# Kernel optimization log

Hardware: AMD Instinct MI355X
Metric: run time of the kernel (lower is better)

Reference implementation:

```python
import jax, jax.numpy as jnp
import numpy as np

B, T, D, U = 32, 2048, 1024, 1024

def setup_inputs() -> dict:
    key = jax.random.key(0)
    ks = jax.random.split(key, 6)
    scale = 1.0 / np.sqrt(D)
    return {
        "features": jax.random.normal(ks[0], (B, T, D), dtype=jnp.float32),
        "hidden": jax.random.normal(ks[1], (B, D), dtype=jnp.float32),
        "W1": jax.random.normal(ks[2], (D, U), dtype=jnp.float32) * scale,
        "b1": jnp.zeros((U,), dtype=jnp.float32),
        "W2": jax.random.normal(ks[3], (D, U), dtype=jnp.float32) * scale,
        "b2": jnp.zeros((U,), dtype=jnp.float32),
        "V": jax.random.normal(ks[4], (U, 1), dtype=jnp.float32) * (1.0 / np.sqrt(U)),
        "bV": jnp.zeros((1,), dtype=jnp.float32),
    }

def reference(features, hidden, W1, b1, W2, b2, V, bV):
    # features: [B,T,D], hidden: [B,D]
    proj_f = jnp.einsum('btd,du->btu', features, W1) + b1          # [B,T,U]
    proj_h = (hidden @ W2 + b2)[:, None, :]                        # [B,1,U]
    score = jnp.tanh(proj_f + proj_h)                              # [B,T,U]
    logits = jnp.einsum('btu,uo->bto', score, V) + bV              # [B,T,1]
    attention_weights = jax.nn.softmax(logits, axis=1)             # [B,T,1]
    context_vector = jnp.sum(attention_weights * features, axis=1) # [B,D]
    return context_vector, attention_weights
```

## Files before the change

### kernel.cpp

```cpp
#include <hip/hip_runtime.h>
#include <hip/hip_bf16.h>
#include <hip/hip_fp16.h>

#define B_ 32
#define T_ 2048
#define D_ 1024
#define U_ 1024
#define M_ (B_ * T_)
#define NT_ 4

typedef _Float16 f16x8 __attribute__((ext_vector_type(8)));
typedef _Float16 f16x4 __attribute__((ext_vector_type(4)));
typedef float f32x4 __attribute__((ext_vector_type(4)));

__device__ __forceinline__ float fast_tanh(float x) {
    float xc = fminf(fmaxf(x, -10.f), 10.f);
    float e = __expf(2.f * xc);
    return 1.f - 2.f / (e + 1.f);
}

__device__ __forceinline__ void load_lds16(const void* g, void* l) {
    __builtin_amdgcn_global_load_lds(
        (const __attribute__((address_space(1))) void*)g,
        (__attribute__((address_space(3))) void*)l, 16, 0, 0);
}

__global__ void precast_kernel(const float* __restrict__ in,
                               _Float16* __restrict__ out) {
    size_t i = (size_t)blockIdx.x * 256 + threadIdx.x;
    const size_t stride = (size_t)2048 * 256;
    const size_t n8 = (size_t)M_ * D_ / 8;
    for (size_t j = i; j < n8; j += stride) {
        f32x4 a = *(const f32x4*)(in + j * 8);
        f32x4 b = *(const f32x4*)(in + j * 8 + 4);
        f16x8 h;
        h[0] = (_Float16)a[0]; h[1] = (_Float16)a[1];
        h[2] = (_Float16)a[2]; h[3] = (_Float16)a[3];
        h[4] = (_Float16)b[0]; h[5] = (_Float16)b[1];
        h[6] = (_Float16)b[2]; h[7] = (_Float16)b[3];
        *(f16x8*)(out + j * 8) = h;
    }
}

__global__ void transpose_cast_kernel(const float* __restrict__ W1,
                                      _Float16* __restrict__ W1t) {
    int u = blockIdx.x * 256 + threadIdx.x;
    int d0 = blockIdx.y * 64;
    for (int j8 = 0; j8 < 8; ++j8) {
        f16x8 h;
        #pragma unroll
        for (int j = 0; j < 8; ++j)
            h[j] = (_Float16)W1[(size_t)(d0 + j8 * 8 + j) * U_ + u];
        *(f16x8*)&W1t[(size_t)u * D_ + d0 + j8 * 8] = h;
    }
}

__global__ void proj_h_partial_kernel(const float* __restrict__ hidden,
                                      const float* __restrict__ W2,
                                      float* __restrict__ pph) {
    int u = blockIdx.x * 256 + threadIdx.x;
    int c = blockIdx.y;
    __shared__ float hb[32][128];
    for (int i = threadIdx.x; i < 32 * 128; i += 256)
        hb[i >> 7][i & 127] = hidden[(i >> 7) * D_ + c * 128 + (i & 127)];
    __syncthreads();
    float acc[32] = {};
    for (int d = 0; d < 128; ++d) {
        float w = W2[(size_t)(c * 128 + d) * U_ + u];
        #pragma unroll
        for (int b = 0; b < 32; ++b) acc[b] = fmaf(hb[b][d], w, acc[b]);
    }
    #pragma unroll
    for (int b = 0; b < 32; ++b)
        pph[((size_t)c * 32 + b) * U_ + u] = acc[b];
}

__global__ void proj_h_combine_kernel(const float* __restrict__ pph,
                                      const float* __restrict__ b1,
                                      const float* __restrict__ b2,
                                      float* __restrict__ ph) {
    int u = blockIdx.x * 256 + threadIdx.x;
    float bias = b1[u] + b2[u];
    for (int b = 0; b < 32; ++b) {
        float s = bias;
        #pragma unroll
        for (int c = 0; c < 8; ++c) s += pph[((size_t)c * 32 + b) * U_ + u];
        ph[b * U_ + u] = s;
    }
}


#define VM4 asm volatile("s_waitcnt vmcnt(4)" ::: "memory");
#define VM0 asm volatile("s_waitcnt vmcnt(0)" ::: "memory");

#define STAGE_A(bb, kh, kof) \
    load_lds16(pA + (kof) + (kh) * 64, sb + (bb) * 65536 + (kh) * 16384 + tid * 16); \
    load_lds16(pA + (size_t)128 * D_ * 2 + (kof) + (kh) * 64, \
               sb + (bb) * 65536 + (kh) * 16384 + 8192 + tid * 16);
#define STAGE_B(bb, kh, kof) \
    load_lds16(pB + (kof) + (kh) * 64, sb + (bb) * 65536 + 32768 + (kh) * 16384 + tid * 16); \
    load_lds16(pB + (size_t)128 * D_ * 2 + (kof) + (kh) * 64, \
               sb + (bb) * 65536 + 32768 + (kh) * 16384 + 8192 + tid * 16);

#define PH(curv, kh, mh, STG, WAITV) do { \
    const char* base_ = sb + (curv) * 65536 + (kh) * 16384; \
    if ((mh) == 0) { \
        _Pragma("unroll") \
        for (int n_ = 0; n_ < 4; ++n_) \
            bf[n_] = *(const f16x8*)(base_ + 32768 + wc * 4096 + n_ * 1024 + laneOff); \
    } \
    _Pragma("unroll") \
    for (int m_ = 0; m_ < 4; ++m_) \
        af[m_] = *(const f16x8*)(base_ + wr * 8192 + (mh) * 4096 + m_ * 1024 + laneOff); \
    STG \
    __builtin_amdgcn_sched_barrier(0); \
    WAITV \
    __builtin_amdgcn_sched_barrier(0); \
    __builtin_amdgcn_s_barrier(); \
    asm volatile("s_waitcnt lgkmcnt(0)" ::: "memory"); \
    __builtin_amdgcn_sched_barrier(0); \
    __builtin_amdgcn_s_setprio(1); \
    _Pragma("unroll") \
    for (int m_ = 0; m_ < 4; ++m_) { \
        _Pragma("unroll") \
        for (int n_ = 0; n_ < 4; ++n_) \
            acc[(mh) * 4 + m_][n_] = __builtin_amdgcn_mfma_f32_16x16x32_f16( \
                af[m_], bf[n_], acc[(mh) * 4 + m_][n_], 0, 0, 0); \
    } \
    __builtin_amdgcn_s_setprio(0); \
    __builtin_amdgcn_sched_barrier(0); \
    __builtin_amdgcn_s_barrier(); \
    __builtin_amdgcn_sched_barrier(0); \
} while (0)

__global__ __launch_bounds__(512, 2)
void gemm_logits_8ph_kernel(const _Float16* __restrict__ A,
                            const _Float16* __restrict__ Bt,
                            const float* __restrict__ ph,
                            const float* __restrict__ V,
                            float* __restrict__ part)
{
    __shared__ __align__(16) char smem_raw[131072];
    char* sb = smem_raw;

    int bid = blockIdx.x;
    int xcd = bid & 7, local = bid >> 3;
    int mt = xcd * 32 + (local >> 2);
    int nt = local & 3;

    int tid = threadIdx.x;
    int l = tid & 63, wid = tid >> 6;
    int wr = wid >> 2, wc = wid & 3;
    int lrow = l & 15;

    const _Float16* Ag = A + (size_t)mt * 256 * D_;
    const _Float16* Bg = Bt + (size_t)nt * 256 * D_;

    int srow = tid >> 2;
    int chunk = (tid & 3) ^ ((srow >> 1) & 3);
    size_t rb = (size_t)srow * (D_ * 2) + (size_t)chunk * 16;
    const char* pA = (const char*)Ag + rb;
    const char* pB = (const char*)Bg + rb;

    int laneOff = lrow * 64 + (((l >> 4) ^ ((lrow >> 1) & 3)) << 4);

    f32x4 acc[8][4] = {};
    f16x8 af[4], bf[4];

    STAGE_A(0, 0, 0)
    STAGE_B(0, 0, 0)
    STAGE_A(0, 1, 0)
    STAGE_B(0, 1, 0)
    VM4
    __builtin_amdgcn_s_barrier();
    __builtin_amdgcn_sched_barrier(0);

    #pragma unroll 1
    for (int t = 0; t < 15; ++t) {
        int cur = t & 1, nxt = cur ^ 1;
        int kof = (t + 1) * 128;
        PH(cur, 0, 0, STAGE_A(nxt, 0, kof), );
        PH(cur, 0, 1, STAGE_B(nxt, 0, kof), VM4);
        PH(cur, 1, 0, STAGE_A(nxt, 1, kof), );
        PH(cur, 1, 1, STAGE_B(nxt, 1, kof), VM4);
    }
    PH(1, 0, 0, , );
    PH(1, 0, 1, , VM0);
    PH(1, 1, 0, , );
    PH(1, 1, 1, , );

    int bidx = mt >> 3;
    const float* phb = ph + bidx * U_;
    float Vv[4], phv[4];
    #pragma unroll
    for (int n = 0; n < 4; ++n) {
        int u = nt * 256 + wc * 64 + n * 16 + lrow;
        Vv[n] = V[u];
        phv[n] = phb[u];
    }
    float* lbuf = (float*)smem_raw;
    #pragma unroll
    for (int mh = 0; mh < 2; ++mh) {
        #pragma unroll
        for (int m = 0; m < 4; ++m) {
            #pragma unroll
            for (int r = 0; r < 4; ++r) {
                float p = 0.f;
                #pragma unroll
                for (int n = 0; n < 4; ++n) {
                    float s = fast_tanh(acc[mh * 4 + m][n][r] + phv[n]);
                    p = fmaf(s, Vv[n], p);
                }
                #pragma unroll
                for (int off = 1; off < 16; off <<= 1)
                    p += __shfl_xor(p, off, 64);
                if (lrow == 0) {
                    int row = wr * 128 + mh * 64 + m * 16 + ((l >> 4) << 2) + r;
                    lbuf[wc * 256 + row] = p;
                }
            }
        }
    }
    __syncthreads();
    if (tid < 256) {
        float v = lbuf[tid] + lbuf[256 + tid] + lbuf[512 + tid] + lbuf[768 + tid];
        part[(size_t)nt * M_ + mt * 256 + tid] = v;
    }
}

__global__ void softmax_kernel(const float* __restrict__ part,
                               float* __restrict__ wout) {
    int b = blockIdx.x;
    int tid = threadIdx.x;
    __shared__ float red[8];
    float lg[8];
    #pragma unroll
    for (int j = 0; j < 8; ++j) {
        int t = tid + j * 256;
        float s = 0.f;
        #pragma unroll
        for (int p = 0; p < NT_; ++p)
            s += part[(size_t)p * M_ + b * T_ + t];
        lg[j] = s;
    }
    float mx = lg[0];
    #pragma unroll
    for (int j = 1; j < 8; ++j) mx = fmaxf(mx, lg[j]);
    #pragma unroll
    for (int off = 1; off < 64; off <<= 1) mx = fmaxf(mx, __shfl_xor(mx, off, 64));
    int wv = tid >> 6;
    if ((tid & 63) == 0) red[wv] = mx;
    __syncthreads();
    mx = fmaxf(fmaxf(red[0], red[1]), fmaxf(red[2], red[3]));
    float e[8];
    float sum = 0.f;
    #pragma unroll
    for (int j = 0; j < 8; ++j) { e[j] = __expf(lg[j] - mx); sum += e[j]; }
    #pragma unroll
    for (int off = 1; off < 64; off <<= 1) sum += __shfl_xor(sum, off, 64);
    if ((tid & 63) == 0) red[4 + wv] = sum;
    __syncthreads();
    sum = red[4] + red[5] + red[6] + red[7];
    float inv = 1.f / sum;
    #pragma unroll
    for (int j = 0; j < 8; ++j)
        wout[b * T_ + tid + j * 256] = e[j] * inv;
}

#define TCH 128
__global__ void context_partial_f16_kernel(const _Float16* __restrict__ feats,
                                           const float* __restrict__ w,
                                           float* __restrict__ cpart) {
    int b = blockIdx.x, tc = blockIdx.y, tid = threadIdx.x;
    f32x4 acc = {0.f, 0.f, 0.f, 0.f};
    const _Float16* f = feats + ((size_t)b * T_ + tc * TCH) * D_ + tid * 4;
    const float* wp = w + b * T_ + tc * TCH;
    #pragma unroll 4
    for (int t = 0; t < TCH; ++t) {
        float wt = wp[t];
        f16x4 fv = *(const f16x4*)(f + (size_t)t * D_);
        acc[0] = fmaf(wt, (float)fv[0], acc[0]);
        acc[1] = fmaf(wt, (float)fv[1], acc[1]);
        acc[2] = fmaf(wt, (float)fv[2], acc[2]);
        acc[3] = fmaf(wt, (float)fv[3], acc[3]);
    }
    *(f32x4*)&cpart[((size_t)tc * B_ + b) * D_ + tid * 4] = acc;
}

__global__ void context_reduce_kernel(const float* __restrict__ cpart,
                                      float* __restrict__ out) {
    int i = blockIdx.x * 256 + threadIdx.x;
    float s = 0.f;
    #pragma unroll
    for (int tc = 0; tc < 16; ++tc)
        s += cpart[(size_t)tc * (B_ * D_) + i];
    out[i] = s;
}

extern "C" void kernel_launch(void* const* d_in, const int* in_sizes, int n_in,
                              void* d_out, int out_size, void* d_ws, size_t ws_size,
                              hipStream_t stream) {
    const float* features = (const float*)d_in[0];
    const float* hidden   = (const float*)d_in[1];
    const float* W1       = (const float*)d_in[2];
    const float* b1       = (const float*)d_in[3];
    const float* W2       = (const float*)d_in[4];
    const float* b2       = (const float*)d_in[5];
    const float* V        = (const float*)d_in[6];

    float* ctx_out = (float*)d_out;
    float* w_out   = ctx_out + B_ * D_;

    char* ws = (char*)d_ws;
    _Float16* W1t  = (_Float16*)ws;
    float* ph      = (float*)(ws + (size_t)(2 << 20));
    float* pph     = (float*)(ws + (size_t)(3 << 20));
    float* part    = (float*)(ws + (size_t)(4 << 20));
    float* cpart   = (float*)(ws + (size_t)(6 << 20));
    _Float16* featH = (_Float16*)(ws + (size_t)(8 << 20));

    transpose_cast_kernel<<<dim3(4, 16), 256, 0, stream>>>(W1, W1t);
    proj_h_partial_kernel<<<dim3(4, 8), 256, 0, stream>>>(hidden, W2, pph);
    proj_h_combine_kernel<<<4, 256, 0, stream>>>(pph, b1, b2, ph);
    precast_kernel<<<2048, 256, 0, stream>>>(features, featH);

    gemm_logits_8ph_kernel<<<(M_ / 256) * (U_ / 256), 512, 0, stream>>>(
        featH, W1t, ph, V, part);

    softmax_kernel<<<B_, 256, 0, stream>>>(part, w_out);
    context_partial_f16_kernel<<<dim3(B_, 16), 256, 0, stream>>>(featH, w_out, cpart);
    context_reduce_kernel<<<(B_ * D_) / 256, 256, 0, stream>>>(cpart, ctx_out);
}
```

Before: 318.4 us.

## Fuse fp32-to-fp16 feature cast into GEMM A-tile loading and drop precast

Removes the separate precast kernel that wrote an fp16 copy of the features. The GEMM now loads fp32 features into registers, converts them to fp16 and writes them into swizzled LDS, while W1t is still loaded asynchronously into LDS. The main loop is restructured into one double-buffered 64-wide K step per iteration with a single barrier. The context kernel now reads the fp32 features directly. This saves the precast's full read and write pass, but doubles the bytes read by the context kernel and adds register staging and conversion work inside the GEMM, which may weaken load/compute overlap.

```diff
diff --git a/kernel.cpp b/kernel.cpp
--- a/kernel.cpp
+++ b/kernel.cpp
@@ -10,7 +10,6 @@
 #define NT_ 4
 
 typedef _Float16 f16x8 __attribute__((ext_vector_type(8)));
-typedef _Float16 f16x4 __attribute__((ext_vector_type(4)));
 typedef float f32x4 __attribute__((ext_vector_type(4)));
 
 __device__ __forceinline__ float fast_tanh(float x) {
@@ -23,23 +22,6 @@
     __builtin_amdgcn_global_load_lds(
         (const __attribute__((address_space(1))) void*)g,
         (__attribute__((address_space(3))) void*)l, 16, 0, 0);
-}
-
-__global__ void precast_kernel(const float* __restrict__ in,
-                               _Float16* __restrict__ out) {
-    size_t i = (size_t)blockIdx.x * 256 + threadIdx.x;
-    const size_t stride = (size_t)2048 * 256;
-    const size_t n8 = (size_t)M_ * D_ / 8;
-    for (size_t j = i; j < n8; j += stride) {
-        f32x4 a = *(const f32x4*)(in + j * 8);
-        f32x4 b = *(const f32x4*)(in + j * 8 + 4);
-        f16x8 h;
-        h[0] = (_Float16)a[0]; h[1] = (_Float16)a[1];
-        h[2] = (_Float16)a[2]; h[3] = (_Float16)a[3];
-        h[4] = (_Float16)b[0]; h[5] = (_Float16)b[1];
-        h[6] = (_Float16)b[2]; h[7] = (_Float16)b[3];
-        *(f16x8*)(out + j * 8) = h;
-    }
 }
 
 __global__ void transpose_cast_kernel(const float* __restrict__ W1,
@@ -90,58 +72,46 @@
 }
 
 
-#define VM4 asm volatile("s_waitcnt vmcnt(4)" ::: "memory");
-#define VM0 asm volatile("s_waitcnt vmcnt(0)" ::: "memory");
-
-#define STAGE_A(bb, kh, kof) \
-    load_lds16(pA + (kof) + (kh) * 64, sb + (bb) * 65536 + (kh) * 16384 + tid * 16); \
-    load_lds16(pA + (size_t)128 * D_ * 2 + (kof) + (kh) * 64, \
-               sb + (bb) * 65536 + (kh) * 16384 + 8192 + tid * 16);
-#define STAGE_B(bb, kh, kof) \
-    load_lds16(pB + (kof) + (kh) * 64, sb + (bb) * 65536 + 32768 + (kh) * 16384 + tid * 16); \
-    load_lds16(pB + (size_t)128 * D_ * 2 + (kof) + (kh) * 64, \
-               sb + (bb) * 65536 + 32768 + (kh) * 16384 + 8192 + tid * 16);
-
-#define PH(curv, kh, mh, STG, WAITV) do { \
-    const char* base_ = sb + (curv) * 65536 + (kh) * 16384; \
-    if ((mh) == 0) { \
-        _Pragma("unroll") \
-        for (int n_ = 0; n_ < 4; ++n_) \
-            bf[n_] = *(const f16x8*)(base_ + 32768 + wc * 4096 + n_ * 1024 + laneOff); \
-    } \
-    _Pragma("unroll") \
-    for (int m_ = 0; m_ < 4; ++m_) \
-        af[m_] = *(const f16x8*)(base_ + wr * 8192 + (mh) * 4096 + m_ * 1024 + laneOff); \
-    STG \
-    __builtin_amdgcn_sched_barrier(0); \
-    WAITV \
-    __builtin_amdgcn_sched_barrier(0); \
-    __builtin_amdgcn_s_barrier(); \
-    asm volatile("s_waitcnt lgkmcnt(0)" ::: "memory"); \
-    __builtin_amdgcn_sched_barrier(0); \
-    __builtin_amdgcn_s_setprio(1); \
-    _Pragma("unroll") \
-    for (int m_ = 0; m_ < 4; ++m_) { \
-        _Pragma("unroll") \
-        for (int n_ = 0; n_ < 4; ++n_) \
-            acc[(mh) * 4 + m_][n_] = __builtin_amdgcn_mfma_f32_16x16x32_f16( \
-                af[m_], bf[n_], acc[(mh) * 4 + m_][n_], 0, 0, 0); \
-    } \
-    __builtin_amdgcn_s_setprio(0); \
-    __builtin_amdgcn_sched_barrier(0); \
-    __builtin_amdgcn_s_barrier(); \
-    __builtin_amdgcn_sched_barrier(0); \
+#define ISSUE_A(koff) do { \
+    const float* a0_ = pA0 + (koff); \
+    const float* a1_ = pA1 + (koff); \
+    araw0 = *(const f32x4*)(a0_);      araw1 = *(const f32x4*)(a0_ + 4); \
+    araw2 = *(const f32x4*)(a0_ + 8);  araw3 = *(const f32x4*)(a0_ + 12); \
+    araw4 = *(const f32x4*)(a1_);      araw5 = *(const f32x4*)(a1_ + 4); \
+    araw6 = *(const f32x4*)(a1_ + 8);  araw7 = *(const f32x4*)(a1_ + 12); \
 } while (0)
 
+#define ISSUE_B(koffb, bufoff) do { \
+    load_lds16(pB + 0 * 131072 + (koffb), smem + (bufoff) + 32768 + 0 * 8192 + tid * 16); \
+    load_lds16(pB + 1 * 131072 + (koffb), smem + (bufoff) + 32768 + 1 * 8192 + tid * 16); \
+    load_lds16(pB + 2 * 131072 + (koffb), smem + (bufoff) + 32768 + 2 * 8192 + tid * 16); \
+    load_lds16(pB + 3 * 131072 + (koffb), smem + (bufoff) + 32768 + 3 * 8192 + tid * 16); \
+} while (0)
+
+#define WRITE_A(nbptr) do { \
+    f16x8 h0_, h1_, h2_, h3_; \
+    h0_[0]=(_Float16)araw0[0]; h0_[1]=(_Float16)araw0[1]; h0_[2]=(_Float16)araw0[2]; h0_[3]=(_Float16)araw0[3]; \
+    h0_[4]=(_Float16)araw1[0]; h0_[5]=(_Float16)araw1[1]; h0_[6]=(_Float16)araw1[2]; h0_[7]=(_Float16)araw1[3]; \
+    h1_[0]=(_Float16)araw2[0]; h1_[1]=(_Float16)araw2[1]; h1_[2]=(_Float16)araw2[2]; h1_[3]=(_Float16)araw2[3]; \
+    h1_[4]=(_Float16)araw3[0]; h1_[5]=(_Float16)araw3[1]; h1_[6]=(_Float16)araw3[2]; h1_[7]=(_Float16)araw3[3]; \
+    h2_[0]=(_Float16)araw4[0]; h2_[1]=(_Float16)araw4[1]; h2_[2]=(_Float16)araw4[2]; h2_[3]=(_Float16)araw4[3]; \
+    h2_[4]=(_Float16)araw5[0]; h2_[5]=(_Float16)araw5[1]; h2_[6]=(_Float16)araw5[2]; h2_[7]=(_Float16)araw5[3]; \
+    h3_[0]=(_Float16)araw6[0]; h3_[1]=(_Float16)araw6[1]; h3_[2]=(_Float16)araw6[2]; h3_[3]=(_Float16)araw6[3]; \
+    h3_[4]=(_Float16)araw7[0]; h3_[5]=(_Float16)araw7[1]; h3_[6]=(_Float16)araw7[2]; h3_[7]=(_Float16)araw7[3]; \
+    *(f16x8*)((nbptr) + aw00) = h0_; \
+    *(f16x8*)((nbptr) + aw01) = h1_; \
+    *(f16x8*)((nbptr) + aw10) = h2_; \
+    *(f16x8*)((nbptr) + aw11) = h3_; \
+} while (0)
+
 __global__ __launch_bounds__(512, 2)
-void gemm_logits_8ph_kernel(const _Float16* __restrict__ A,
-                            const _Float16* __restrict__ Bt,
-                            const float* __restrict__ ph,
-                            const float* __restrict__ V,
-                            float* __restrict__ part)
+void gemm_logits_v4_kernel(const float* __restrict__ A,
+                           const _Float16* __restrict__ Bt,
+                           const float* __restrict__ ph,
+                           const float* __restrict__ V,
+                           float* __restrict__ part)
 {
-    __shared__ __align__(16) char smem_raw[131072];
-    char* sb = smem_raw;
+    __shared__ __align__(16) char smem[131072];
 
     int bid = blockIdx.x;
     int xcd = bid & 7, local = bid >> 3;
@@ -151,43 +121,78 @@
     int tid = threadIdx.x;
     int l = tid & 63, wid = tid >> 6;
     int wr = wid >> 2, wc = wid & 3;
-    int lrow = l & 15;
-
-    const _Float16* Ag = A + (size_t)mt * 256 * D_;
+    int lrow = l & 15, lksl = l >> 4;
+
+    const float* Ag = A + (size_t)mt * 256 * D_;
     const _Float16* Bg = Bt + (size_t)nt * 256 * D_;
 
-    int srow = tid >> 2;
-    int chunk = (tid & 3) ^ ((srow >> 1) & 3);
-    size_t rb = (size_t)srow * (D_ * 2) + (size_t)chunk * 16;
-    const char* pA = (const char*)Ag + rb;
-    const char* pB = (const char*)Bg + rb;
-
-    int laneOff = lrow * 64 + (((l >> 4) ^ ((lrow >> 1) & 3)) << 4);
+    const float* pA0 = Ag + (size_t)(tid >> 2) * D_ + (tid & 3) * 16;
+    const float* pA1 = pA0 + (size_t)128 * D_;
+    int c2 = (tid & 3) * 2;
+    int r0 = tid >> 2;
+    int sw = r0 & 7;
+    int aw00 = r0 * 128 + ((c2 ^ sw) << 4);
+    int aw01 = r0 * 128 + (((c2 | 1) ^ sw) << 4);
+    int aw10 = (r0 + 128) * 128 + ((c2 ^ sw) << 4);
+    int aw11 = (r0 + 128) * 128 + (((c2 | 1) ^ sw) << 4);
+
+    int bchunk = (tid & 7) ^ ((tid >> 3) & 7);
+    const char* pB = (const char*)Bg + (size_t)(tid >> 3) * 2048 + bchunk * 16;
+
+    int rowA = (wr * 128 + lrow) * 128;
+    int rowB = 32768 + (wc * 64 + lrow) * 128;
+    int sw7 = lrow & 7;
 
     f32x4 acc[8][4] = {};
-    f16x8 af[4], bf[4];
-
-    STAGE_A(0, 0, 0)
-    STAGE_B(0, 0, 0)
-    STAGE_A(0, 1, 0)
-    STAGE_B(0, 1, 0)
-    VM4
+    f32x4 araw0, araw1, araw2, araw3, araw4, araw5, araw6, araw7;
+
+    ISSUE_A(0);
+    ISSUE_B(0, 0);
+    WRITE_A(smem);
+    __builtin_amdgcn_sched_barrier(0);
+    asm volatile("s_waitcnt vmcnt(0)" ::: "memory");
+    asm volatile("s_waitcnt lgkmcnt(0)" ::: "memory");
+    __builtin_amdgcn_sched_barrier(0);
     __builtin_amdgcn_s_barrier();
     __builtin_amdgcn_sched_barrier(0);
 
     #pragma unroll 1
-    for (int t = 0; t < 15; ++t) {
-        int cur = t & 1, nxt = cur ^ 1;
-        int kof = (t + 1) * 128;
-        PH(cur, 0, 0, STAGE_A(nxt, 0, kof), );
-        PH(cur, 0, 1, STAGE_B(nxt, 0, kof), VM4);
-        PH(cur, 1, 0, STAGE_A(nxt, 1, kof), );
-        PH(cur, 1, 1, STAGE_B(nxt, 1, kof), VM4);
-    }
-    PH(1, 0, 0, , );
-    PH(1, 0, 1, , VM0);
-    PH(1, 1, 0, , );
-    PH(1, 1, 1, , );
+    for (int t = 0; t < 16; ++t) {
+        const char* bb = smem + (t & 1) * 65536;
+        char* nb = smem + ((t & 1) ^ 1) * 65536;
+        if (t < 15) {
+            ISSUE_A((t + 1) * 64);
+            ISSUE_B((t + 1) * 128, ((t & 1) ^ 1) * 65536);
+        }
+        __builtin_amdgcn_s_setprio(1);
+        #pragma unroll
+        for (int kh = 0; kh < 2; ++kh) {
+            int us = (((kh << 2) | lksl) ^ sw7) << 4;
+            f16x8 af[8], bf[4];
+            #pragma unroll
+            for (int n = 0; n < 4; ++n)
+                bf[n] = *(const f16x8*)(bb + rowB + n * 2048 + us);
+            #pragma unroll
+            for (int m = 0; m < 8; ++m)
+                af[m] = *(const f16x8*)(bb + rowA + m * 2048 + us);
+            #pragma unroll
+            for (int m = 0; m < 8; ++m)
+                #pragma unroll
+                for (int n = 0; n < 4; ++n)
+                    acc[m][n] = __builtin_amdgcn_mfma_f32_16x16x32_f16(
+                        af[m], bf[n], acc[m][n], 0, 0, 0);
+        }
+        __builtin_amdgcn_s_setprio(0);
+        if (t < 15) {
+            WRITE_A(nb);
+            __builtin_amdgcn_sched_barrier(0);
+            asm volatile("s_waitcnt vmcnt(0)" ::: "memory");
+            asm volatile("s_waitcnt lgkmcnt(0)" ::: "memory");
+            __builtin_amdgcn_sched_barrier(0);
+            __builtin_amdgcn_s_barrier();
+            __builtin_amdgcn_sched_barrier(0);
+        }
+    }
 
     int bidx = mt >> 3;
     const float* phb = ph + bidx * U_;
@@ -198,26 +203,23 @@
         Vv[n] = V[u];
         phv[n] = phb[u];
     }
-    float* lbuf = (float*)smem_raw;
-    #pragma unroll
-    for (int mh = 0; mh < 2; ++mh) {
-        #pragma unroll
-        for (int m = 0; m < 4; ++m) {
-            #pragma unroll
-            for (int r = 0; r < 4; ++r) {
-                float p = 0.f;
-                #pragma unroll
-                for (int n = 0; n < 4; ++n) {
-                    float s = fast_tanh(acc[mh * 4 + m][n][r] + phv[n]);
-                    p = fmaf(s, Vv[n], p);
-                }
-                #pragma unroll
-                for (int off = 1; off < 16; off <<= 1)
-                    p += __shfl_xor(p, off, 64);
-                if (lrow == 0) {
-                    int row = wr * 128 + mh * 64 + m * 16 + ((l >> 4) << 2) + r;
-                    lbuf[wc * 256 + row] = p;
-                }
+    float* lbuf = (float*)smem;
+    #pragma unroll
+    for (int m = 0; m < 8; ++m) {
+        #pragma unroll
+        for (int r = 0; r < 4; ++r) {
+            float p = 0.f;
+            #pragma unroll
+            for (int n = 0; n < 4; ++n) {
+                float s = fast_tanh(acc[m][n][r] + phv[n]);
+                p = fmaf(s, Vv[n], p);
+            }
+            #pragma unroll
+            for (int off = 1; off < 16; off <<= 1)
+                p += __shfl_xor(p, off, 64);
+            if (lrow == 0) {
+                int row = wr * 128 + m * 16 + ((l >> 4) << 2) + r;
+                lbuf[wc * 256 + row] = p;
             }
         }
     }
@@ -268,21 +270,20 @@
 }
 
 #define TCH 128
-__global__ void context_partial_f16_kernel(const _Float16* __restrict__ feats,
-                                           const float* __restrict__ w,
-                                           float* __restrict__ cpart) {
+__global__ void context_partial_kernel(const float* __restrict__ feats,
+                                       const float* __restrict__ w,
+                                       float* __restrict__ cpart) {
     int b = blockIdx.x, tc = blockIdx.y, tid = threadIdx.x;
     f32x4 acc = {0.f, 0.f, 0.f, 0.f};
-    const _Float16* f = feats + ((size_t)b * T_ + tc * TCH) * D_ + tid * 4;
+    const float* f = feats + ((size_t)b * T_ + tc * TCH) * D_ + tid * 4;
     const float* wp = w + b * T_ + tc * TCH;
-    #pragma unroll 4
     for (int t = 0; t < TCH; ++t) {
         float wt = wp[t];
-        f16x4 fv = *(const f16x4*)(f + (size_t)t * D_);
-        acc[0] = fmaf(wt, (float)fv[0], acc[0]);
-        acc[1] = fmaf(wt, (float)fv[1], acc[1]);
-        acc[2] = fmaf(wt, (float)fv[2], acc[2]);
-        acc[3] = fmaf(wt, (float)fv[3], acc[3]);
+        f32x4 fv = *(const f32x4*)(f + (size_t)t * D_);
+        acc[0] = fmaf(wt, fv[0], acc[0]);
+        acc[1] = fmaf(wt, fv[1], acc[1]);
+        acc[2] = fmaf(wt, fv[2], acc[2]);
+        acc[3] = fmaf(wt, fv[3], acc[3]);
     }
     *(f32x4*)&cpart[((size_t)tc * B_ + b) * D_ + tid * 4] = acc;
 }
@@ -312,22 +313,20 @@
     float* w_out   = ctx_out + B_ * D_;
 
     char* ws = (char*)d_ws;
-    _Float16* W1t  = (_Float16*)ws;
-    float* ph      = (float*)(ws + (size_t)(2 << 20));
-    float* pph     = (float*)(ws + (size_t)(3 << 20));
-    float* part    = (float*)(ws + (size_t)(4 << 20));
-    float* cpart   = (float*)(ws + (size_t)(6 << 20));
-    _Float16* featH = (_Float16*)(ws + (size_t)(8 << 20));
+    _Float16* W1t = (_Float16*)ws;
+    float* ph     = (float*)(ws + (size_t)(2 << 20));
+    float* pph    = (float*)(ws + (size_t)(3 << 20));
+    float* part   = (float*)(ws + (size_t)(4 << 20));
+    float* cpart  = (float*)(ws + (size_t)(6 << 20));
 
     transpose_cast_kernel<<<dim3(4, 16), 256, 0, stream>>>(W1, W1t);
     proj_h_partial_kernel<<<dim3(4, 8), 256, 0, stream>>>(hidden, W2, pph);
     proj_h_combine_kernel<<<4, 256, 0, stream>>>(pph, b1, b2, ph);
-    precast_kernel<<<2048, 256, 0, stream>>>(features, featH);
-
-    gemm_logits_8ph_kernel<<<(M_ / 256) * (U_ / 256), 512, 0, stream>>>(
-        featH, W1t, ph, V, part);
+
+    gemm_logits_v4_kernel<<<(M_ / 256) * (U_ / 256), 512, 0, stream>>>(
+        features, W1t, ph, V, part);
 
     softmax_kernel<<<B_, 256, 0, stream>>>(part, w_out);
-    context_partial_f16_kernel<<<dim3(B_, 16), 256, 0, stream>>>(featH, w_out, cpart);
+    context_partial_kernel<<<dim3(B_, 16), 256, 0, stream>>>(features, w_out, cpart);
     context_reduce_kernel<<<(B_ * D_) / 256, 256, 0, stream>>>(cpart, ctx_out);
 }
```

New measurement: 297.1 us. 1.07x faster.

## Pre-swizzle features and W1 into MFMA fragment layout, keep W1 slice resident in LDS

Applied to the files above, without the earlier changes.

Features and W1 are cast to fp16 and stored in a tiled layout that matches the MFMA 16x16x32 operand fragments. Each GEMM block now keeps a 64-column slice of W1 resident in LDS for the whole K range, while A fragments are loaded straight from global memory into registers with software double-buffering. Because block output tiles narrow from 256 to 64 columns, NT_ grows to 16 partial logit rows. The context kernel reads the same tiled layout and reduces with shuffles, which removes the separate context reduce kernel. This drops the per-K-step LDS staging and barriers for A, but each A tile is re-read from global memory by 16 column blocks, and occupancy is limited by the large LDS buffer.

```diff
diff --git a/kernel.cpp b/kernel.cpp
--- a/kernel.cpp
+++ b/kernel.cpp
@@ -7,10 +7,9 @@
 #define D_ 1024
 #define U_ 1024
 #define M_ (B_ * T_)
-#define NT_ 4
+#define NT_ 16
 
 typedef _Float16 f16x8 __attribute__((ext_vector_type(8)));
-typedef _Float16 f16x4 __attribute__((ext_vector_type(4)));
 typedef float f32x4 __attribute__((ext_vector_type(4)));
 
 __device__ __forceinline__ float fast_tanh(float x) {
@@ -25,33 +24,38 @@
         (__attribute__((address_space(3))) void*)l, 16, 0, 0);
 }
 
-__global__ void precast_kernel(const float* __restrict__ in,
-                               _Float16* __restrict__ out) {
-    size_t i = (size_t)blockIdx.x * 256 + threadIdx.x;
-    const size_t stride = (size_t)2048 * 256;
-    const size_t n8 = (size_t)M_ * D_ / 8;
-    for (size_t j = i; j < n8; j += stride) {
-        f32x4 a = *(const f32x4*)(in + j * 8);
-        f32x4 b = *(const f32x4*)(in + j * 8 + 4);
+__global__ void precastT_kernel(const float* __restrict__ in,
+                                _Float16* __restrict__ out) {
+    int mt = blockIdx.x;
+    int t = threadIdx.x;
+    int slot = t & 15, kb0 = t >> 4;
+    const float* src = in + ((size_t)mt * 16 + slot) * D_;
+    _Float16* dst = out + (size_t)mt * 16384 + slot * 8;
+    #pragma unroll
+    for (int i = 0; i < 8; ++i) {
+        int kb = kb0 + i * 16;
+        f32x4 a = *(const f32x4*)(src + kb * 8);
+        f32x4 b = *(const f32x4*)(src + kb * 8 + 4);
         f16x8 h;
         h[0] = (_Float16)a[0]; h[1] = (_Float16)a[1];
         h[2] = (_Float16)a[2]; h[3] = (_Float16)a[3];
         h[4] = (_Float16)b[0]; h[5] = (_Float16)b[1];
         h[6] = (_Float16)b[2]; h[7] = (_Float16)b[3];
-        *(f16x8*)(out + j * 8) = h;
-    }
-}
-
-__global__ void transpose_cast_kernel(const float* __restrict__ W1,
-                                      _Float16* __restrict__ W1t) {
+        *(f16x8*)(dst + kb * 128) = h;
+    }
+}
+
+__global__ void transpose_cast_W1T_kernel(const float* __restrict__ W1,
+                                          _Float16* __restrict__ W1T) {
     int u = blockIdx.x * 256 + threadIdx.x;
     int d0 = blockIdx.y * 64;
+    _Float16* dst = W1T + (size_t)(u >> 4) * 16384 + (u & 15) * 8;
     for (int j8 = 0; j8 < 8; ++j8) {
         f16x8 h;
         #pragma unroll
         for (int j = 0; j < 8; ++j)
             h[j] = (_Float16)W1[(size_t)(d0 + j8 * 8 + j) * U_ + u];
-        *(f16x8*)&W1t[(size_t)u * D_ + d0 + j8 * 8] = h;
+        *(f16x8*)(dst + (size_t)(d0 / 8 + j8) * 128) = h;
     }
 }
 
@@ -90,141 +94,111 @@
 }
 
 
-#define VM4 asm volatile("s_waitcnt vmcnt(4)" ::: "memory");
-#define VM0 asm volatile("s_waitcnt vmcnt(0)" ::: "memory");
-
-#define STAGE_A(bb, kh, kof) \
-    load_lds16(pA + (kof) + (kh) * 64, sb + (bb) * 65536 + (kh) * 16384 + tid * 16); \
-    load_lds16(pA + (size_t)128 * D_ * 2 + (kof) + (kh) * 64, \
-               sb + (bb) * 65536 + (kh) * 16384 + 8192 + tid * 16);
-#define STAGE_B(bb, kh, kof) \
-    load_lds16(pB + (kof) + (kh) * 64, sb + (bb) * 65536 + 32768 + (kh) * 16384 + tid * 16); \
-    load_lds16(pB + (size_t)128 * D_ * 2 + (kof) + (kh) * 64, \
-               sb + (bb) * 65536 + 32768 + (kh) * 16384 + 8192 + tid * 16);
-
-#define PH(curv, kh, mh, STG, WAITV) do { \
-    const char* base_ = sb + (curv) * 65536 + (kh) * 16384; \
-    if ((mh) == 0) { \
+#define LOAD_AF(dst, mtb, s) do { \
+    const char* a_ = fT + ((size_t)(mtb) << 15) + (s) * 1024 + l16; \
+    _Pragma("unroll") \
+    for (int m_ = 0; m_ < 8; ++m_) \
+        dst[m_] = *(const f16x8*)(a_ + (m_ << 15)); \
+} while (0)
+
+#define READ_BF(s) do { \
+    _Pragma("unroll") \
+    for (int n_ = 0; n_ < 4; ++n_) \
+        bfc[n_] = *(const f16x8*)(lB + n_ * 32768 + (s) * 1024 + l16); \
+} while (0)
+
+#define MFMA_STEP(AF) do { \
+    __builtin_amdgcn_s_setprio(1); \
+    _Pragma("unroll") \
+    for (int m_ = 0; m_ < 8; ++m_) \
         _Pragma("unroll") \
         for (int n_ = 0; n_ < 4; ++n_) \
-            bf[n_] = *(const f16x8*)(base_ + 32768 + wc * 4096 + n_ * 1024 + laneOff); \
-    } \
-    _Pragma("unroll") \
-    for (int m_ = 0; m_ < 4; ++m_) \
-        af[m_] = *(const f16x8*)(base_ + wr * 8192 + (mh) * 4096 + m_ * 1024 + laneOff); \
-    STG \
-    __builtin_amdgcn_sched_barrier(0); \
-    WAITV \
-    __builtin_amdgcn_sched_barrier(0); \
-    __builtin_amdgcn_s_barrier(); \
-    asm volatile("s_waitcnt lgkmcnt(0)" ::: "memory"); \
-    __builtin_amdgcn_sched_barrier(0); \
-    __builtin_amdgcn_s_setprio(1); \
-    _Pragma("unroll") \
-    for (int m_ = 0; m_ < 4; ++m_) { \
-        _Pragma("unroll") \
-        for (int n_ = 0; n_ < 4; ++n_) \
-            acc[(mh) * 4 + m_][n_] = __builtin_amdgcn_mfma_f32_16x16x32_f16( \
-                af[m_], bf[n_], acc[(mh) * 4 + m_][n_], 0, 0, 0); \
-    } \
+            acc[m_][n_] = __builtin_amdgcn_mfma_f32_16x16x32_f16( \
+                AF[m_], bfc[n_], acc[m_][n_], 0, 0, 0); \
     __builtin_amdgcn_s_setprio(0); \
-    __builtin_amdgcn_sched_barrier(0); \
-    __builtin_amdgcn_s_barrier(); \
-    __builtin_amdgcn_sched_barrier(0); \
 } while (0)
 
 __global__ __launch_bounds__(512, 2)
-void gemm_logits_8ph_kernel(const _Float16* __restrict__ A,
-                            const _Float16* __restrict__ Bt,
-                            const float* __restrict__ ph,
-                            const float* __restrict__ V,
-                            float* __restrict__ part)
+void gemm_logits_v7_kernel(const _Float16* __restrict__ featT,
+                           const _Float16* __restrict__ W1T,
+                           const float* __restrict__ ph,
+                           const float* __restrict__ V,
+                           float* __restrict__ part)
 {
-    __shared__ __align__(16) char smem_raw[131072];
-    char* sb = smem_raw;
+    __shared__ __align__(16) _Float16 Bs[65536];
 
     int bid = blockIdx.x;
     int xcd = bid & 7, local = bid >> 3;
-    int mt = xcd * 32 + (local >> 2);
-    int nt = local & 3;
+    int mtcg = xcd * 2 + (local >> 4);
+    int nt = local & 15;
 
     int tid = threadIdx.x;
-    int l = tid & 63, wid = tid >> 6;
-    int wr = wid >> 2, wc = wid & 3;
-    int lrow = l & 15;
-
-    const _Float16* Ag = A + (size_t)mt * 256 * D_;
-    const _Float16* Bg = Bt + (size_t)nt * 256 * D_;
-
-    int srow = tid >> 2;
-    int chunk = (tid & 3) ^ ((srow >> 1) & 3);
-    size_t rb = (size_t)srow * (D_ * 2) + (size_t)chunk * 16;
-    const char* pA = (const char*)Ag + rb;
-    const char* pB = (const char*)Bg + rb;
-
-    int laneOff = lrow * 64 + (((l >> 4) ^ ((lrow >> 1) & 3)) << 4);
-
+    int l = tid & 63, w = tid >> 6;
+    int l16 = l * 16;
+    const char* fT = (const char*)featT;
+    const char* lB = (const char*)Bs;
+
+    {
+        const char* src = (const char*)W1T + (size_t)nt * 131072;
+        #pragma unroll
+        for (int i = 0; i < 16; ++i)
+            load_lds16(src + i * 8192 + tid * 16, (char*)Bs + i * 8192 + tid * 16);
+    }
+
+    f16x8 afA[8], afB[8], bfc[4];
     f32x4 acc[8][4] = {};
-    f16x8 af[4], bf[4];
-
-    STAGE_A(0, 0, 0)
-    STAGE_B(0, 0, 0)
-    STAGE_A(0, 1, 0)
-    STAGE_B(0, 1, 0)
-    VM4
+
+    LOAD_AF(afA, mtcg * 256 + w * 8, 0);
+
+    float Vv[4];
+    #pragma unroll
+    for (int n = 0; n < 4; ++n) Vv[n] = V[nt * 64 + n * 16 + (l & 15)];
+
+    asm volatile("s_waitcnt vmcnt(0)" ::: "memory");
     __builtin_amdgcn_s_barrier();
-    __builtin_amdgcn_sched_barrier(0);
 
     #pragma unroll 1
-    for (int t = 0; t < 15; ++t) {
-        int cur = t & 1, nxt = cur ^ 1;
-        int kof = (t + 1) * 128;
-        PH(cur, 0, 0, STAGE_A(nxt, 0, kof), );
-        PH(cur, 0, 1, STAGE_B(nxt, 0, kof), VM4);
-        PH(cur, 1, 0, STAGE_A(nxt, 1, kof), );
-        PH(cur, 1, 1, STAGE_B(nxt, 1, kof), VM4);
-    }
-    PH(1, 0, 0, , );
-    PH(1, 0, 1, , VM0);
-    PH(1, 1, 0, , );
-    PH(1, 1, 1, , );
-
-    int bidx = mt >> 3;
-    const float* phb = ph + bidx * U_;
-    float Vv[4], phv[4];
-    #pragma unroll
-    for (int n = 0; n < 4; ++n) {
-        int u = nt * 256 + wc * 64 + n * 16 + lrow;
-        Vv[n] = V[u];
-        phv[n] = phb[u];
-    }
-    float* lbuf = (float*)smem_raw;
-    #pragma unroll
-    for (int mh = 0; mh < 2; ++mh) {
-        #pragma unroll
-        for (int m = 0; m < 4; ++m) {
+    for (int c = 0; c < 4; ++c) {
+        int mtb = mtcg * 256 + c * 64 + w * 8;
+        int mtbn = (c < 3) ? (mtb + 64) : mtb;
+
+        #pragma unroll 1
+        for (int s = 0; s < 32; s += 2) {
+            READ_BF(s);
+            LOAD_AF(afB, mtb, s + 1);
+            MFMA_STEP(afA);
+            READ_BF(s + 1);
+            if (s < 30) LOAD_AF(afA, mtb, s + 2);
+            else        LOAD_AF(afA, mtbn, 0);
+            MFMA_STEP(afB);
+        }
+
+        int row0 = mtcg * 4096 + c * 1024 + w * 128;
+        const float* phb = ph + (row0 >> 11) * U_;
+        float phv[4];
+        #pragma unroll
+        for (int n = 0; n < 4; ++n) phv[n] = phb[nt * 64 + n * 16 + (l & 15)];
+        #pragma unroll
+        for (int m = 0; m < 8; ++m) {
             #pragma unroll
             for (int r = 0; r < 4; ++r) {
                 float p = 0.f;
                 #pragma unroll
-                for (int n = 0; n < 4; ++n) {
-                    float s = fast_tanh(acc[mh * 4 + m][n][r] + phv[n]);
-                    p = fmaf(s, Vv[n], p);
-                }
-                #pragma unroll
-                for (int off = 1; off < 16; off <<= 1)
-                    p += __shfl_xor(p, off, 64);
-                if (lrow == 0) {
-                    int row = wr * 128 + mh * 64 + m * 16 + ((l >> 4) << 2) + r;
-                    lbuf[wc * 256 + row] = p;
-                }
+                for (int n = 0; n < 4; ++n)
+                    p = fmaf(fast_tanh(acc[m][n][r] + phv[n]), Vv[n], p);
+                p += __shfl_xor(p, 1, 64);
+                p += __shfl_xor(p, 2, 64);
+                p += __shfl_xor(p, 4, 64);
+                p += __shfl_xor(p, 8, 64);
+                if ((l & 15) == 0)
+                    part[(size_t)nt * M_ + row0 + m * 16 + (l >> 4) * 4 + r] = p;
             }
         }
-    }
-    __syncthreads();
-    if (tid < 256) {
-        float v = lbuf[tid] + lbuf[256 + tid] + lbuf[512 + tid] + lbuf[768 + tid];
-        part[(size_t)nt * M_ + mt * 256 + tid] = v;
+        #pragma unroll
+        for (int m = 0; m < 8; ++m)
+            #pragma unroll
+            for (int n = 0; n < 4; ++n)
+                acc[m][n] = (f32x4){0.f, 0.f, 0.f, 0.f};
     }
 }
 
@@ -267,34 +241,38 @@
         wout[b * T_ + tid + j * 256] = e[j] * inv;
 }
 
-#define TCH 128
-__global__ void context_partial_f16_kernel(const _Float16* __restrict__ feats,
-                                           const float* __restrict__ w,
-                                           float* __restrict__ cpart) {
-    int b = blockIdx.x, tc = blockIdx.y, tid = threadIdx.x;
-    f32x4 acc = {0.f, 0.f, 0.f, 0.f};
-    const _Float16* f = feats + ((size_t)b * T_ + tc * TCH) * D_ + tid * 4;
-    const float* wp = w + b * T_ + tc * TCH;
+__global__ void context_v7_kernel(const _Float16* __restrict__ featT,
+                                  const float* __restrict__ w,
+                                  float* __restrict__ ctx) {
+    int b = blockIdx.x;
+    int dc = blockIdx.y;
+    int t = threadIdx.x;
+    __shared__ float wLds[2048];
+    for (int i = t; i < 2048; i += 256) wLds[i] = w[b * T_ + i];
+    __syncthreads();
+
+    float acc[8] = {};
+    const char* base = (const char*)featT + (size_t)b * 128 * 32768 + dc * 4096 + t * 16;
+    int slot = t & 15;
     #pragma unroll 4
-    for (int t = 0; t < TCH; ++t) {
-        float wt = wp[t];
-        f16x4 fv = *(const f16x4*)(f + (size_t)t * D_);
-        acc[0] = fmaf(wt, (float)fv[0], acc[0]);
-        acc[1] = fmaf(wt, (float)fv[1], acc[1]);
-        acc[2] = fmaf(wt, (float)fv[2], acc[2]);
-        acc[3] = fmaf(wt, (float)fv[3], acc[3]);
-    }
-    *(f32x4*)&cpart[((size_t)tc * B_ + b) * D_ + tid * 4] = acc;
-}
-
-__global__ void context_reduce_kernel(const float* __restrict__ cpart,
-                                      float* __restrict__ out) {
-    int i = blockIdx.x * 256 + threadIdx.x;
-    float s = 0.f;
-    #pragma unroll
-    for (int tc = 0; tc < 16; ++tc)
-        s += cpart[(size_t)tc * (B_ * D_) + i];
-    out[i] = s;
+    for (int mt = 0; mt < 128; ++mt) {
+        f16x8 v = *(const f16x8*)(base + (size_t)mt * 32768);
+        float wt = wLds[mt * 16 + slot];
+        #pragma unroll
+        for (int j = 0; j < 8; ++j) acc[j] = fmaf(wt, (float)v[j], acc[j]);
+    }
+    #pragma unroll
+    for (int j = 0; j < 8; ++j) {
+        acc[j] += __shfl_xor(acc[j], 1, 64);
+        acc[j] += __shfl_xor(acc[j], 2, 64);
+        acc[j] += __shfl_xor(acc[j], 4, 64);
+        acc[j] += __shfl_xor(acc[j], 8, 64);
+    }
+    if ((t & 15) == 0) {
+        float* o = ctx + b * D_ + dc * 128 + (t >> 4) * 8;
+        #pragma unroll
+        for (int j = 0; j < 8; ++j) o[j] = acc[j];
+    }
 }
 
 extern "C" void kernel_launch(void* const* d_in, const int* in_sizes, int n_in,
@@ -312,22 +290,19 @@
     float* w_out   = ctx_out + B_ * D_;
 
     char* ws = (char*)d_ws;
-    _Float16* W1t  = (_Float16*)ws;
+    _Float16* W1T  = (_Float16*)ws;
     float* ph      = (float*)(ws + (size_t)(2 << 20));
-    float* pph     = (float*)(ws + (size_t)(3 << 20));
+    float* pph     = (float*)(ws + (size_t)(2 << 20) + (1 << 17));
     float* part    = (float*)(ws + (size_t)(4 << 20));
-    float* cpart   = (float*)(ws + (size_t)(6 << 20));
-    _Float16* featH = (_Float16*)(ws + (size_t)(8 << 20));
-
-    transpose_cast_kernel<<<dim3(4, 16), 256, 0, stream>>>(W1, W1t);
+    _Float16* featT = (_Float16*)(ws + (size_t)(8 << 20));
+
+    transpose_cast_W1T_kernel<<<dim3(4, 16), 256, 0, stream>>>(W1, W1T);
     proj_h_partial_kernel<<<dim3(4, 8), 256, 0, stream>>>(hidden, W2, pph);
     proj_h_combine_kernel<<<4, 256, 0, stream>>>(pph, b1, b2, ph);
-    precast_kernel<<<2048, 256, 0, stream>>>(features, featH);
-
-    gemm_logits_8ph_kernel<<<(M_ / 256) * (U_ / 256), 512, 0, stream>>>(
-        featH, W1t, ph, V, part);
+    precastT_kernel<<<4096, 256, 0, stream>>>(features, featT);
+
+    gemm_logits_v7_kernel<<<256, 512, 0, stream>>>(featT, W1T, ph, V, part);
 
     softmax_kernel<<<B_, 256, 0, stream>>>(part, w_out);
-    context_partial_f16_kernel<<<dim3(B_, 16), 256, 0, stream>>>(featH, w_out, cpart);
-    context_reduce_kernel<<<(B_ * D_) / 256, 256, 0, stream>>>(cpart, ctx_out);
-}
+    context_v7_kernel<<<dim3(B_, 8), 256, 0, stream>>>(featT, w_out, ctx_out);
+}
```

New measurement: 324.5 us. About the same (+1.9%).
